# Kernel optimization log

Hardware: AMD Instinct MI355X
Metric: run time of the kernel (lower is better)

## Reference

```python
import jax, jax.numpy as jnp
import numpy as np

N_NODES = 50000
N_EDGES = 1600000
IN_FEAT = 256
HIDDEN = 128
N_CLASSES = 16


def gcn_conv(x, edge_index, W, b, n_nodes):
    """PyG GCNConv: x' = D^{-1/2} (A+I) D^{-1/2} (x @ W) + b."""
    h = x @ W  # project first (PyG order), messages are in out_dim
    src, dst = edge_index[0], edge_index[1]
    loops = jnp.arange(n_nodes, dtype=src.dtype)
    src = jnp.concatenate([src, loops])
    dst = jnp.concatenate([dst, loops])
    # degree of A+I (count incoming edges incl. self loop)
    deg = jax.ops.segment_sum(jnp.ones_like(dst, dtype=h.dtype), dst, num_segments=n_nodes)
    dis = jax.lax.rsqrt(deg)  # deg >= 1 thanks to self loops
    norm = dis[src] * dis[dst]  # [E+N]
    msgs = h[src] * norm[:, None]  # gather + scale
    out = jax.ops.segment_sum(msgs, dst, num_segments=n_nodes)  # scatter-add
    return out + b


def setup_inputs() -> dict:
    key = jax.random.key(0)
    k_x, k_e, k_w1, k_b1, k_w2, k_b2 = jax.random.split(key, 6)
    x = jax.random.normal(k_x, (N_NODES, IN_FEAT), dtype=jnp.float32)
    edge_index = jax.random.randint(k_e, (2, N_EDGES), 0, N_NODES, dtype=jnp.int64)
    s1 = 1.0 / np.sqrt(IN_FEAT)
    s2 = 1.0 / np.sqrt(HIDDEN)
    W1 = jax.random.uniform(k_w1, (IN_FEAT, HIDDEN), jnp.float32, -s1, s1)
    b1 = jax.random.uniform(k_b1, (HIDDEN,), jnp.float32, -s1, s1)
    W2 = jax.random.uniform(k_w2, (HIDDEN, N_CLASSES), jnp.float32, -s2, s2)
    b2 = jax.random.uniform(k_b2, (N_CLASSES,), jnp.float32, -s2, s2)
    return {"x": x, "edge_index": edge_index, "W1": W1, "b1": b1, "W2": W2, "b2": b2}


def reference(x, edge_index, W1, b1, W2, b2):
    n = x.shape[0]
    h = gcn_conv(x, edge_index, W1, b1, n)
    h = jax.nn.relu(h)
    logits = gcn_conv(h, edge_index, W2, b2, n)
    return logits, jax.nn.softmax(logits, axis=1)
```

## Files before the change

### kernel.cpp

```cpp
#include <hip/hip_runtime.h>
#include <hip/hip_bf16.h>
#include <math.h>

#define N_NODES 50000
#define N_EDGES 1600000
#define IN_FEAT 256
#define HIDDEN 128
#define N_CLASSES 16

#define ECHUNK 2048
#define NCHK 782
#define NBKT 196
#define BCAP 10240
#define CSTR 16

typedef __attribute__((ext_vector_type(8))) short short8;
typedef __attribute__((ext_vector_type(4))) float floatx4;

__device__ __forceinline__ unsigned short f2bf(float f) {
    unsigned u = __float_as_uint(f);
    return (unsigned short)((u + 0x7fffu + ((u >> 16) & 1u)) >> 16);
}

__device__ __forceinline__ unsigned pk2bf(float a, float b) {
    __hip_bfloat162 h = __float22bfloat162_rn(make_float2(a, b));
    union { __hip_bfloat162 h; unsigned u; } cv;
    cv.h = h;
    return cv.u;
}

__device__ __forceinline__ float bflo(unsigned u) { return __uint_as_float(u << 16); }
__device__ __forceinline__ float bfhi(unsigned u) { return __uint_as_float(u & 0xffff0000u); }

__global__ __launch_bounds__(256) void scatter_edges2(const int* __restrict__ src,
                                                      const int* __restrict__ dst,
                                                      int* __restrict__ cursor,
                                                      unsigned int* __restrict__ sorted,
                                                      const float* __restrict__ W1,
                                                      unsigned short* __restrict__ w1t) {
    __shared__ int hloc[256];
    int t = threadIdx.x;
    hloc[t] = 0;
    if (blockIdx.x < HIDDEN)
        w1t[blockIdx.x * IN_FEAT + t] = f2bf(W1[t * HIDDEN + blockIdx.x]);
    __syncthreads();
    int base = blockIdx.x * ECHUNK;
    int end = min(base + ECHUNK, N_EDGES);
    for (int i = base + t; i < end; i += 256)
        atomicAdd(&hloc[dst[i] >> 8], 1);
    __syncthreads();
    int cnt = hloc[t];
    int lbase = 0;
    if (cnt > 0) lbase = t * BCAP + atomicAdd(&cursor[t * CSTR], cnt);
    __syncthreads();
    hloc[t] = lbase;
    __syncthreads();
    for (int i = base + t; i < end; i += 256) {
        int d = dst[i];
        int s = src[i];
        int pos = atomicAdd(&hloc[d >> 8], 1);
        sorted[pos] = ((unsigned)d << 16) | (unsigned)s;
    }
}

__global__ __launch_bounds__(512) void build_csr2(const unsigned int* __restrict__ sorted,
                                                  const int* __restrict__ cursor,
                                                  int* __restrict__ rs,
                                                  int* __restrict__ re,
                                                  float* __restrict__ dis,
                                                  unsigned short* __restrict__ csr_src) {
    __shared__ int cnt[256];
    __shared__ int roff[256];
    int t = threadIdx.x;
    int bkt = blockIdx.x;
    int ebase = bkt * BCAP;
    int eend = ebase + cursor[bkt * CSTR];
    if (t < 256) cnt[t] = 0;
    __syncthreads();
    for (int i = ebase + t; i < eend; i += 512)
        atomicAdd(&cnt[(sorted[i] >> 16) & 255], 1);
    __syncthreads();
    int v = 0;
    if (t < 256) { v = cnt[t]; roff[t] = v; }
    __syncthreads();
    for (int off = 1; off < 256; off <<= 1) {
        int x = (t < 256 && t >= off) ? roff[t - off] : 0;
        __syncthreads();
        if (t < 256) roff[t] += x;
        __syncthreads();
    }
    if (t < 256) {
        int excl = roff[t] - v;
        int node = bkt * 256 + t;
        if (node < N_NODES) {
            rs[node] = ebase + excl;
            re[node] = ebase + excl + v;
            dis[node] = 1.0f / sqrtf((float)(v + 1));
        }
        cnt[t] = ebase + excl;
    }
    __syncthreads();
    for (int i = ebase + t; i < eend; i += 512) {
        unsigned e = sorted[i];
        int pos = atomicAdd(&cnt[(e >> 16) & 255], 1);
        csr_src[pos] = (unsigned short)(e & 0xffffu);
    }
}

#define XCH 260

__global__ __launch_bounds__(256) void gemm1_mfma(const float* __restrict__ x,
                                                  const unsigned short* __restrict__ w1t,
                                                  const float* __restrict__ dis,
                                                  unsigned int* __restrict__ g1) {
    __shared__ float xs[2][8 * XCH];
    int tid = threadIdx.x;
    int w = tid >> 6;
    int lane = tid & 63;
    int quad = lane >> 4;
    int c = lane & 15;
    int row_base = blockIdx.x * 64;
    int wrow = (w >> 1) * 32;
    int col_base = (w & 1) * 64;

    int st_row = min(row_base + 16 * w + (lane >> 3), N_NODES - 1);
    int st_row2 = min(row_base + 16 * w + 8 + (lane >> 3), N_NODES - 1);
    const float* gp1 = x + (size_t)st_row * IN_FEAT + (lane & 7) * 4;
    const float* gp2 = x + (size_t)st_row2 * IN_FEAT + (lane & 7) * 4;

    floatx4 acc[2][4] = {};
    const unsigned short* bp[4];
#pragma unroll
    for (int nt = 0; nt < 4; ++nt)
        bp[nt] = w1t + (size_t)(col_base + nt * 16 + c) * IN_FEAT + quad * 8;

    int dwoff[2];
#pragma unroll
    for (int rt = 0; rt < 2; ++rt) {
        int rit = wrow + rt * 16 + c;
        dwoff[rt] = (rit >> 3) * XCH + (rit & 7) * 32 + quad * 8;
    }

#define STAGE(buf, k0)                                                                  \
    do {                                                                                \
        __builtin_amdgcn_global_load_lds(                                               \
            (const __attribute__((address_space(1))) void*)(gp1 + (k0)),                \
            (__attribute__((address_space(3))) void*)&xs[buf][(2 * w) * XCH], 16, 0, 0);\
        __builtin_amdgcn_global_load_lds(                                               \
            (const __attribute__((address_space(1))) void*)(gp2 + (k0)),                \
            (__attribute__((address_space(3))) void*)&xs[buf][(2 * w + 1) * XCH], 16, 0, 0);\
    } while (0)

    STAGE(0, 0);
    __syncthreads();

    int buf = 0;
#pragma unroll
    for (int kk = 0; kk < 8; ++kk) {
        if (kk < 7) STAGE(buf ^ 1, (kk + 1) * 32);
        short8 b[4];
#pragma unroll
        for (int nt = 0; nt < 4; ++nt)
            b[nt] = *(const short8*)(bp[nt] + kk * 32);
        short8 a[2];
#pragma unroll
        for (int rt = 0; rt < 2; ++rt) {
            float4 f0 = *(const float4*)&xs[buf][dwoff[rt]];
            float4 f1 = *(const float4*)&xs[buf][dwoff[rt] + 4];
            union { short8 s; unsigned u[4]; } au;
            au.u[0] = pk2bf(f0.x, f0.y);
            au.u[1] = pk2bf(f0.z, f0.w);
            au.u[2] = pk2bf(f1.x, f1.y);
            au.u[3] = pk2bf(f1.z, f1.w);
            a[rt] = au.s;
        }
#pragma unroll
        for (int rt = 0; rt < 2; ++rt)
#pragma unroll
            for (int nt = 0; nt < 4; ++nt)
                acc[rt][nt] = __builtin_amdgcn_mfma_f32_16x16x32_bf16(a[rt], b[nt], acc[rt][nt], 0, 0, 0);
        __syncthreads();
        buf ^= 1;
    }
#undef STAGE

    bool evenlane = (lane & 1) == 0;
#pragma unroll
    for (int rt = 0; rt < 2; ++rt) {
#pragma unroll
        for (int reg = 0; reg < 4; ++reg) {
            int row = row_base + wrow + rt * 16 + quad * 4 + reg;
            float dv = dis[min(row, N_NODES - 1)];
#pragma unroll
            for (int nt = 0; nt < 4; ++nt) {
                float v = acc[rt][nt][reg] * dv;
                float vo = __shfl_xor(v, 1);
                if (evenlane && row < N_NODES) {
                    unsigned pkd = (unsigned)f2bf(v) | ((unsigned)f2bf(vo) << 16);
                    int col = col_base + nt * 16 + c;
                    g1[(size_t)(col >> 5) * (N_NODES * 16) + (size_t)row * 16 + ((col & 31) >> 1)] = pkd;
                }
            }
        }
    }
}

__global__ __launch_bounds__(256) void agg1_sliced(const uint4* __restrict__ g1,
                                                   const int* __restrict__ rs,
                                                   const int* __restrict__ re,
                                                   const unsigned short* __restrict__ csr_src,
                                                   const float* __restrict__ dis,
                                                   const float* __restrict__ b1,
                                                   const float* __restrict__ W2,
                                                   float* __restrict__ g2p) {
    __shared__ float w2s[32 * 16];
    __shared__ float rbuf[4][16][36];
    int tid = threadIdx.x;
    int bi = blockIdx.x;
    int bucket = bi >> 4;
    int xcd = bi & 7;
    int slice = xcd >> 1;
    int quarter = ((bi >> 3) & 1) * 2 + (xcd & 1);

    for (int i = tid; i < 512; i += 256) w2s[i] = W2[slice * 512 + i];
    __syncthreads();

    int wave = tid >> 6, lane = tid & 63;
    int g = lane >> 2, m4 = lane & 3;
    const uint4* plane = g1 + (size_t)slice * (N_NODES * 4);
    float* gp = g2p + (size_t)slice * ((size_t)N_NODES * 16);
    int node = bucket * 256 + quarter * 64 + wave * 16 + g;
    bool alive = (node < N_NODES);

#define ACC8(u) do { a0 += bflo((u).x); a1 += bfhi((u).x); a2 += bflo((u).y); a3 += bfhi((u).y); \
                     a4 += bflo((u).z); a5 += bfhi((u).z); a6 += bflo((u).w); a7 += bfhi((u).w); } while (0)
#define GATH(IV, U0, U1, U2, U3) do {                       \
        int j0_ = (int)((IV).x & 0xffffu);                  \
        int j1_ = (int)((IV).x >> 16);                      \
        int j2_ = (int)((IV).y & 0xffffu);                  \
        int j3_ = (int)((IV).y >> 16);                      \
        U0 = plane[(size_t)j0_ * 4 + m4];                   \
        U1 = plane[(size_t)j1_ * 4 + m4];                   \
        U2 = plane[(size_t)j2_ * 4 + m4];                   \
        U3 = plane[(size_t)j3_ * 4 + m4];                   \
    } while (0)

    if (alive) {
        uint4 su = plane[(size_t)node * 4 + m4];
        float a0 = bflo(su.x), a1 = bfhi(su.x), a2 = bflo(su.y), a3 = bfhi(su.y);
        float a4 = bflo(su.z), a5 = bfhi(su.z), a6 = bflo(su.w), a7 = bfhi(su.w);
        int e = rs[node], e1v = re[node];
        while ((e & 3) && e < e1v) {
            int j = csr_src[e];
            uint4 u = plane[(size_t)j * 4 + m4];
            ACC8(u);
            ++e;
        }
        int nb = (e1v - e) >> 2;
        if (nb >= 2) {
            uint2 Ia = *(const uint2*)&csr_src[e];
            uint2 Ib = *(const uint2*)&csr_src[e + 4];
            uint4 A0, A1, A2, A3, B0, B1, B2, B3;
            GATH(Ia, A0, A1, A2, A3);
            GATH(Ib, B0, B1, B2, B3);
            __builtin_amdgcn_sched_barrier(0);
            int b = 2;
            while (b + 2 <= nb) {
                Ia = *(const uint2*)&csr_src[e + 4 * b];
                ACC8(A0); ACC8(A1); ACC8(A2); ACC8(A3);
                GATH(Ia, A0, A1, A2, A3);
                __builtin_amdgcn_sched_barrier(0);
                Ib = *(const uint2*)&csr_src[e + 4 * b + 4];
                ACC8(B0); ACC8(B1); ACC8(B2); ACC8(B3);
                GATH(Ib, B0, B1, B2, B3);
                __builtin_amdgcn_sched_barrier(0);
                b += 2;
            }
            int rem = nb - b;
            ACC8(A0); ACC8(A1); ACC8(A2); ACC8(A3);
            if (rem) {
                Ia = *(const uint2*)&csr_src[e + 4 * b];
                GATH(Ia, A0, A1, A2, A3);
            }
            ACC8(B0); ACC8(B1); ACC8(B2); ACC8(B3);
            if (rem) { ACC8(A0); ACC8(A1); ACC8(A2); ACC8(A3); }
            e += 4 * nb;
        } else if (nb >= 1) {
            uint2 Iv = *(const uint2*)&csr_src[e];
            uint4 U0, U1, U2, U3;
            GATH(Iv, U0, U1, U2, U3);
            ACC8(U0); ACC8(U1); ACC8(U2); ACC8(U3);
            e += 4;
        }
        while (e < e1v) {
            int j = csr_src[e];
            uint4 u = plane[(size_t)j * 4 + m4];
            ACC8(u);
            ++e;
        }

        float dv = dis[node];
        float4 bb0 = *(const float4*)&b1[slice * 32 + 8 * m4];
        float4 bb1 = *(const float4*)&b1[slice * 32 + 8 * m4 + 4];
        float4 r0, r1;
        r0.x = fmaxf(fmaf(dv, a0, bb0.x), 0.f);
        r0.y = fmaxf(fmaf(dv, a1, bb0.y), 0.f);
        r0.z = fmaxf(fmaf(dv, a2, bb0.z), 0.f);
        r0.w = fmaxf(fmaf(dv, a3, bb0.w), 0.f);
        r1.x = fmaxf(fmaf(dv, a4, bb1.x), 0.f);
        r1.y = fmaxf(fmaf(dv, a5, bb1.y), 0.f);
        r1.z = fmaxf(fmaf(dv, a6, bb1.z), 0.f);
        r1.w = fmaxf(fmaf(dv, a7, bb1.w), 0.f);
        *(float4*)&rbuf[wave][g][8 * m4] = r0;
        *(float4*)&rbuf[wave][g][8 * m4 + 4] = r1;
    }
    __builtin_amdgcn_sched_barrier(0);
    if (alive) {
        float p0 = 0.f, p1 = 0.f, p2 = 0.f, p3 = 0.f;
#pragma unroll
        for (int fb = 0; fb < 8; ++fb) {
            float4 rv = *(const float4*)&rbuf[wave][g][fb * 4];
            float4 w0 = *(const float4*)&w2s[(fb * 4 + 0) * 16 + 4 * m4];
            float4 w1 = *(const float4*)&w2s[(fb * 4 + 1) * 16 + 4 * m4];
            float4 w2 = *(const float4*)&w2s[(fb * 4 + 2) * 16 + 4 * m4];
            float4 w3 = *(const float4*)&w2s[(fb * 4 + 3) * 16 + 4 * m4];
            p0 = fmaf(rv.x, w0.x, p0); p1 = fmaf(rv.x, w0.y, p1);
            p2 = fmaf(rv.x, w0.z, p2); p3 = fmaf(rv.x, w0.w, p3);
            p0 = fmaf(rv.y, w1.x, p0); p1 = fmaf(rv.y, w1.y, p1);
            p2 = fmaf(rv.y, w1.z, p2); p3 = fmaf(rv.y, w1.w, p3);
            p0 = fmaf(rv.z, w2.x, p0); p1 = fmaf(rv.z, w2.y, p1);
            p2 = fmaf(rv.z, w2.z, p2); p3 = fmaf(rv.z, w2.w, p3);
            p0 = fmaf(rv.w, w3.x, p0); p1 = fmaf(rv.w, w3.y, p1);
            p2 = fmaf(rv.w, w3.z, p2); p3 = fmaf(rv.w, w3.w, p3);
        }
        float4 pv; pv.x = p0; pv.y = p1; pv.z = p2; pv.w = p3;
        *(float4*)&gp[(size_t)node * 16 + 4 * m4] = pv;
    }
#undef GATH
#undef ACC8
}

__global__ __launch_bounds__(256) void g2_reduce(float* __restrict__ g2p,
                                                 const float* __restrict__ dis) {
    int i = blockIdx.x * 256 + threadIdx.x;
    if (i >= N_NODES * 4) return;
    const size_t PS = (size_t)N_NODES * 16 / 4;
    const float4* p = (const float4*)g2p;
    float4 a = p[i];
    float4 b = p[i + PS];
    float4 c = p[i + 2 * PS];
    float4 d = p[i + 3 * PS];
    float dv = dis[i >> 2];
    float4 r;
    r.x = dv * ((a.x + b.x) + (c.x + d.x));
    r.y = dv * ((a.y + b.y) + (c.y + d.y));
    r.z = dv * ((a.z + b.z) + (c.z + d.z));
    r.w = dv * ((a.w + b.w) + (c.w + d.w));
    ((float4*)g2p)[i] = r;
}

__global__ __launch_bounds__(256) void agg2_softmax(const float4* __restrict__ g2,
                                                    const int* __restrict__ rs,
                                                    const int* __restrict__ re,
                                                    const unsigned short* __restrict__ csr_src,
                                                    const float* __restrict__ dis,
                                                    const float* __restrict__ b2,
                                                    float* __restrict__ out) {
    int tid = threadIdx.x;
    int wave = tid >> 6, lane = tid & 63;
    int g = lane >> 2, m4 = lane & 3;
    int node = blockIdx.x * 64 + wave * 16 + g;
    if (node >= N_NODES) return;

    float4 acc = g2[(size_t)node * 4 + m4];

#define ACC4(u) do { acc.x += (u).x; acc.y += (u).y; acc.z += (u).z; acc.w += (u).w; } while (0)
#define GATH4(IV, U0, U1, U2, U3) do {                      \
        int j0_ = (int)((IV).x & 0xffffu);                  \
        int j1_ = (int)((IV).x >> 16);                      \
        int j2_ = (int)((IV).y & 0xffffu);                  \
        int j3_ = (int)((IV).y >> 16);                      \
        U0 = g2[(size_t)j0_ * 4 + m4];                      \
        U1 = g2[(size_t)j1_ * 4 + m4];                      \
        U2 = g2[(size_t)j2_ * 4 + m4];                      \
        U3 = g2[(size_t)j3_ * 4 + m4];                      \
    } while (0)

    int e = rs[node], e1v = re[node];
    while ((e & 3) && e < e1v) {
        int j = csr_src[e];
        float4 u = g2[(size_t)j * 4 + m4];
        ACC4(u);
        ++e;
    }
    int nb = (e1v - e) >> 2;
    if (nb >= 2) {
        uint2 Ia = *(const uint2*)&csr_src[e];
        uint2 Ib = *(const uint2*)&csr_src[e + 4];
        float4 A0, A1, A2, A3, B0, B1, B2, B3;
        GATH4(Ia, A0, A1, A2, A3);
        GATH4(Ib, B0, B1, B2, B3);
        __builtin_amdgcn_sched_barrier(0);
        int b = 2;
        while (b + 2 <= nb) {
            Ia = *(const uint2*)&csr_src[e + 4 * b];
            ACC4(A0); ACC4(A1); ACC4(A2); ACC4(A3);
            GATH4(Ia, A0, A1, A2, A3);
            __builtin_amdgcn_sched_barrier(0);
            Ib = *(const uint2*)&csr_src[e + 4 * b + 4];
            ACC4(B0); ACC4(B1); ACC4(B2); ACC4(B3);
            GATH4(Ib, B0, B1, B2, B3);
            __builtin_amdgcn_sched_barrier(0);
            b += 2;
        }
        int rem = nb - b;
        ACC4(A0); ACC4(A1); ACC4(A2); ACC4(A3);
        if (rem) {
            Ia = *(const uint2*)&csr_src[e + 4 * b];
            GATH4(Ia, A0, A1, A2, A3);
        }
        ACC4(B0); ACC4(B1); ACC4(B2); ACC4(B3);
        if (rem) { ACC4(A0); ACC4(A1); ACC4(A2); ACC4(A3); }
        e += 4 * nb;
    } else if (nb >= 1) {
        uint2 Iv = *(const uint2*)&csr_src[e];
        float4 U0, U1, U2, U3;
        GATH4(Iv, U0, U1, U2, U3);
        ACC4(U0); ACC4(U1); ACC4(U2); ACC4(U3);
        e += 4;
    }
    while (e < e1v) {
        int j = csr_src[e];
        float4 u = g2[(size_t)j * 4 + m4];
        ACC4(u);
        ++e;
    }
#undef GATH4
#undef ACC4

    float dv = dis[node];
    float4 bb = *(const float4*)&b2[4 * m4];
    float4 lg;
    lg.x = fmaf(dv, acc.x, bb.x);
    lg.y = fmaf(dv, acc.y, bb.y);
    lg.z = fmaf(dv, acc.z, bb.z);
    lg.w = fmaf(dv, acc.w, bb.w);
    ((float4*)out)[(size_t)node * 4 + m4] = lg;

    float m = fmaxf(fmaxf(lg.x, lg.y), fmaxf(lg.z, lg.w));
    m = fmaxf(m, __shfl_xor(m, 1));
    m = fmaxf(m, __shfl_xor(m, 2));
    float4 ex;
    ex.x = expf(lg.x - m); ex.y = expf(lg.y - m);
    ex.z = expf(lg.z - m); ex.w = expf(lg.w - m);
    float s = (ex.x + ex.y) + (ex.z + ex.w);
    s += __shfl_xor(s, 1);
    s += __shfl_xor(s, 2);
    float inv = 1.0f / s;
    ex.x *= inv; ex.y *= inv; ex.z *= inv; ex.w *= inv;
    ((float4*)out)[(size_t)N_NODES * 4 + (size_t)node * 4 + m4] = ex;
}


extern "C" void kernel_launch(void* const* d_in, const int* in_sizes, int n_in,
                              void* d_out, int out_size, void* d_ws, size_t ws_size,
                              hipStream_t stream) {
    const float* x  = (const float*)d_in[0];
    const int*   ei = (const int*)d_in[1];
    const float* W1 = (const float*)d_in[2];
    const float* b1 = (const float*)d_in[3];
    const float* W2 = (const float*)d_in[4];
    const float* b2 = (const float*)d_in[5];
    float* out = (float*)d_out;

    char* ws = (char*)d_ws;
    size_t off = 0;
    auto alloc = [&](size_t bytes) -> char* {
        char* p = ws + off;
        off = (off + bytes + 511) & ~(size_t)511;
        return p;
    };
    int*   cursor   = (int*)alloc(256 * CSTR * 4);
    float* dis      = (float*)alloc(N_NODES * 4);
    int*   rs       = (int*)alloc(N_NODES * 4);
    int*   re       = (int*)alloc(N_NODES * 4);
    unsigned short* w1t = (unsigned short*)alloc((size_t)HIDDEN * IN_FEAT * 2);
    unsigned short* csr_src = (unsigned short*)alloc((size_t)NBKT * BCAP * 2);
    unsigned int* g1 = (unsigned int*)alloc((size_t)N_NODES * 64 * 4);
    float* g2p      = (float*)alloc(4 * (size_t)N_NODES * N_CLASSES * 4);
    unsigned int* sorted = (unsigned int*)g1;
    (void)ws_size; (void)in_sizes; (void)n_in; (void)out_size;

    const int* src = ei;
    const int* dst = ei + N_EDGES;

    hipMemsetAsync(cursor, 0, 256 * CSTR * 4, stream);
    scatter_edges2<<<NCHK, 256, 0, stream>>>(src, dst, cursor, sorted, W1, w1t);
    build_csr2<<<NBKT, 512, 0, stream>>>(sorted, cursor, rs, re, dis, csr_src);

    gemm1_mfma<<<(N_NODES + 63) / 64, 256, 0, stream>>>(x, w1t, dis, g1);
    agg1_sliced<<<NBKT * 16, 256, 0, stream>>>((const uint4*)g1, rs, re, csr_src, dis, b1, W2, g2p);
    g2_reduce<<<(N_NODES * 4 + 255) / 256, 256, 0, stream>>>(g2p, dis);
    agg2_softmax<<<N_NODES / 64 + 1, 256, 0, stream>>>((const float4*)g2p, rs, re, csr_src, dis, b2, out);
}
```

Measured before the change: 224.3 us.

## Fuse slice reduction into agg1 via atomics and restructure gemm1 tiling

The four per-slice partial layer-2 projections are no longer written to separate planes and summed by a g2_reduce kernel. agg1 now scales by dis and atomically adds straight into one zeroed g2 buffer, cleared by a widened memset. This removes a kernel launch and the 4x partial buffer traffic, at the cost of float atomic contention (4 slices per element) and non-deterministic summation order. Separately, gemm1 now uses 32-row blocks with each wave owning 32 columns, and loads the whole K extent into LDS up front instead of double-buffering with a sync per step.

New measurement: 237.7 us. 1.06x slower.

```diff
diff --git a/kernel.cpp b/kernel.cpp
--- a/kernel.cpp
+++ b/kernel.cpp
@@ -107,66 +107,56 @@
     }
 }
 
-#define XCH 260
+#define XCHDW 260
+#define KBLK (4 * XCHDW)
 
 __global__ __launch_bounds__(256) void gemm1_mfma(const float* __restrict__ x,
                                                   const unsigned short* __restrict__ w1t,
                                                   const float* __restrict__ dis,
                                                   unsigned int* __restrict__ g1) {
-    __shared__ float xs[2][8 * XCH];
+    __shared__ float xs[8 * KBLK];
     int tid = threadIdx.x;
     int w = tid >> 6;
     int lane = tid & 63;
     int quad = lane >> 4;
     int c = lane & 15;
-    int row_base = blockIdx.x * 64;
-    int wrow = (w >> 1) * 32;
-    int col_base = (w & 1) * 64;
-
-    int st_row = min(row_base + 16 * w + (lane >> 3), N_NODES - 1);
-    int st_row2 = min(row_base + 16 * w + 8 + (lane >> 3), N_NODES - 1);
+    int row_base = blockIdx.x * 32;
+    int col_base = w * 32;
+
+    int st_row = min(row_base + 8 * w + (lane >> 3), N_NODES - 1);
     const float* gp1 = x + (size_t)st_row * IN_FEAT + (lane & 7) * 4;
-    const float* gp2 = x + (size_t)st_row2 * IN_FEAT + (lane & 7) * 4;
-
-    floatx4 acc[2][4] = {};
-    const unsigned short* bp[4];
-#pragma unroll
-    for (int nt = 0; nt < 4; ++nt)
+#pragma unroll
+    for (int kk = 0; kk < 8; ++kk)
+        __builtin_amdgcn_global_load_lds(
+            (const __attribute__((address_space(1))) void*)(gp1 + kk * 32),
+            (__attribute__((address_space(3))) void*)&xs[kk * KBLK + w * XCHDW], 16, 0, 0);
+
+    floatx4 acc[2][2] = {};
+    const unsigned short* bp[2];
+#pragma unroll
+    for (int nt = 0; nt < 2; ++nt)
         bp[nt] = w1t + (size_t)(col_base + nt * 16 + c) * IN_FEAT + quad * 8;
 
     int dwoff[2];
 #pragma unroll
     for (int rt = 0; rt < 2; ++rt) {
-        int rit = wrow + rt * 16 + c;
-        dwoff[rt] = (rit >> 3) * XCH + (rit & 7) * 32 + quad * 8;
-    }
-
-#define STAGE(buf, k0)                                                                  \
-    do {                                                                                \
-        __builtin_amdgcn_global_load_lds(                                               \
-            (const __attribute__((address_space(1))) void*)(gp1 + (k0)),                \
-            (__attribute__((address_space(3))) void*)&xs[buf][(2 * w) * XCH], 16, 0, 0);\
-        __builtin_amdgcn_global_load_lds(                                               \
-            (const __attribute__((address_space(1))) void*)(gp2 + (k0)),                \
-            (__attribute__((address_space(3))) void*)&xs[buf][(2 * w + 1) * XCH], 16, 0, 0);\
-    } while (0)
-
-    STAGE(0, 0);
-    __syncthreads();
-
-    int buf = 0;
+        int rit = rt * 16 + c;
+        dwoff[rt] = (rit >> 3) * XCHDW + (rit & 7) * 32 + quad * 8;
+    }
+
+    __syncthreads();
+
 #pragma unroll
     for (int kk = 0; kk < 8; ++kk) {
-        if (kk < 7) STAGE(buf ^ 1, (kk + 1) * 32);
-        short8 b[4];
-#pragma unroll
-        for (int nt = 0; nt < 4; ++nt)
+        short8 b[2];
+#pragma unroll
+        for (int nt = 0; nt < 2; ++nt)
             b[nt] = *(const short8*)(bp[nt] + kk * 32);
         short8 a[2];
 #pragma unroll
         for (int rt = 0; rt < 2; ++rt) {
-            float4 f0 = *(const float4*)&xs[buf][dwoff[rt]];
-            float4 f1 = *(const float4*)&xs[buf][dwoff[rt] + 4];
+            float4 f0 = *(const float4*)&xs[kk * KBLK + dwoff[rt]];
+            float4 f1 = *(const float4*)&xs[kk * KBLK + dwoff[rt] + 4];
             union { short8 s; unsigned u[4]; } au;
             au.u[0] = pk2bf(f0.x, f0.y);
             au.u[1] = pk2bf(f0.z, f0.w);
@@ -177,22 +167,19 @@
 #pragma unroll
         for (int rt = 0; rt < 2; ++rt)
 #pragma unroll
-            for (int nt = 0; nt < 4; ++nt)
+            for (int nt = 0; nt < 2; ++nt)
                 acc[rt][nt] = __builtin_amdgcn_mfma_f32_16x16x32_bf16(a[rt], b[nt], acc[rt][nt], 0, 0, 0);
-        __syncthreads();
-        buf ^= 1;
-    }
-#undef STAGE
+    }
 
     bool evenlane = (lane & 1) == 0;
 #pragma unroll
     for (int rt = 0; rt < 2; ++rt) {
 #pragma unroll
         for (int reg = 0; reg < 4; ++reg) {
-            int row = row_base + wrow + rt * 16 + quad * 4 + reg;
+            int row = row_base + rt * 16 + quad * 4 + reg;
             float dv = dis[min(row, N_NODES - 1)];
 #pragma unroll
-            for (int nt = 0; nt < 4; ++nt) {
+            for (int nt = 0; nt < 2; ++nt) {
                 float v = acc[rt][nt][reg] * dv;
                 float vo = __shfl_xor(v, 1);
                 if (evenlane && row < N_NODES) {
@@ -212,7 +199,7 @@
                                                    const float* __restrict__ dis,
                                                    const float* __restrict__ b1,
                                                    const float* __restrict__ W2,
-                                                   float* __restrict__ g2p) {
+                                                   float* __restrict__ g2) {
     __shared__ float w2s[32 * 16];
     __shared__ float rbuf[4][16][36];
     int tid = threadIdx.x;
@@ -228,9 +215,9 @@
     int wave = tid >> 6, lane = tid & 63;
     int g = lane >> 2, m4 = lane & 3;
     const uint4* plane = g1 + (size_t)slice * (N_NODES * 4);
-    float* gp = g2p + (size_t)slice * ((size_t)N_NODES * 16);
     int node = bucket * 256 + quarter * 64 + wave * 16 + g;
     bool alive = (node < N_NODES);
+    float dvs = 0.f;
 
 #define ACC8(u) do { a0 += bflo((u).x); a1 += bfhi((u).x); a2 += bflo((u).y); a3 += bfhi((u).y); \
                      a4 += bflo((u).z); a5 += bfhi((u).z); a6 += bflo((u).w); a7 += bfhi((u).w); } while (0)
@@ -300,6 +287,7 @@
         }
 
         float dv = dis[node];
+        dvs = dv;
         float4 bb0 = *(const float4*)&b1[slice * 32 + 8 * m4];
         float4 bb1 = *(const float4*)&b1[slice * 32 + 8 * m4 + 4];
         float4 r0, r1;
@@ -333,30 +321,14 @@
             p0 = fmaf(rv.w, w3.x, p0); p1 = fmaf(rv.w, w3.y, p1);
             p2 = fmaf(rv.w, w3.z, p2); p3 = fmaf(rv.w, w3.w, p3);
         }
-        float4 pv; pv.x = p0; pv.y = p1; pv.z = p2; pv.w = p3;
-        *(float4*)&gp[(size_t)node * 16 + 4 * m4] = pv;
+        float* go = g2 + (size_t)node * 16 + 4 * m4;
+        unsafeAtomicAdd(go + 0, dvs * p0);
+        unsafeAtomicAdd(go + 1, dvs * p1);
+        unsafeAtomicAdd(go + 2, dvs * p2);
+        unsafeAtomicAdd(go + 3, dvs * p3);
     }
 #undef GATH
 #undef ACC8
-}
-
-__global__ __launch_bounds__(256) void g2_reduce(float* __restrict__ g2p,
-                                                 const float* __restrict__ dis) {
-    int i = blockIdx.x * 256 + threadIdx.x;
-    if (i >= N_NODES * 4) return;
-    const size_t PS = (size_t)N_NODES * 16 / 4;
-    const float4* p = (const float4*)g2p;
-    float4 a = p[i];
-    float4 b = p[i + PS];
-    float4 c = p[i + 2 * PS];
-    float4 d = p[i + 3 * PS];
-    float dv = dis[i >> 2];
-    float4 r;
-    r.x = dv * ((a.x + b.x) + (c.x + d.x));
-    r.y = dv * ((a.y + b.y) + (c.y + d.y));
-    r.z = dv * ((a.z + b.z) + (c.z + d.z));
-    r.w = dv * ((a.w + b.w) + (c.w + d.w));
-    ((float4*)g2p)[i] = r;
 }
 
 __global__ __launch_bounds__(256) void agg2_softmax(const float4* __restrict__ g2,
@@ -481,25 +453,25 @@
         return p;
     };
     int*   cursor   = (int*)alloc(256 * CSTR * 4);
+    float* g2       = (float*)alloc((size_t)N_NODES * N_CLASSES * 4);
     float* dis      = (float*)alloc(N_NODES * 4);
     int*   rs       = (int*)alloc(N_NODES * 4);
     int*   re       = (int*)alloc(N_NODES * 4);
     unsigned short* w1t = (unsigned short*)alloc((size_t)HIDDEN * IN_FEAT * 2);
     unsigned short* csr_src = (unsigned short*)alloc((size_t)NBKT * BCAP * 2);
     unsigned int* g1 = (unsigned int*)alloc((size_t)N_NODES * 64 * 4);
-    float* g2p      = (float*)alloc(4 * (size_t)N_NODES * N_CLASSES * 4);
     unsigned int* sorted = (unsigned int*)g1;
     (void)ws_size; (void)in_sizes; (void)n_in; (void)out_size;
 
     const int* src = ei;
     const int* dst = ei + N_EDGES;
 
-    hipMemsetAsync(cursor, 0, 256 * CSTR * 4, stream);
+    size_t zspan = (size_t)((char*)(g2 + (size_t)N_NODES * N_CLASSES) - (char*)cursor);
+    hipMemsetAsync(cursor, 0, zspan, stream);
     scatter_edges2<<<NCHK, 256, 0, stream>>>(src, dst, cursor, sorted, W1, w1t);
     build_csr2<<<NBKT, 512, 0, stream>>>(sorted, cursor, rs, re, dis, csr_src);
 
-    gemm1_mfma<<<(N_NODES + 63) / 64, 256, 0, stream>>>(x, w1t, dis, g1);
-    agg1_sliced<<<NBKT * 16, 256, 0, stream>>>((const uint4*)g1, rs, re, csr_src, dis, b1, W2, g2p);
-    g2_reduce<<<(N_NODES * 4 + 255) / 256, 256, 0, stream>>>(g2p, dis);
-    agg2_softmax<<<N_NODES / 64 + 1, 256, 0, stream>>>((const float4*)g2p, rs, re, csr_src, dis, b2, out);
-}
+    gemm1_mfma<<<(N_NODES + 31) / 32, 256, 0, stream>>>(x, w1t, dis, g1);
+    agg1_sliced<<<NBKT * 16, 256, 0, stream>>>((const uint4*)g1, rs, re, csr_src, dis, b1, W2, g2);
+    agg2_softmax<<<N_NODES / 64 + 1, 256, 0, stream>>>((const float4*)g2, rs, re, csr_src, dis, b2, out);
+}
```
